# Kernel tuning notes

Measured on AMD Instinct MI355X. Metric: run time of the kernel, lower is better.

Reference implementation:

```python
import jax, jax.numpy as jnp
import numpy as np

N = 50000      # num nodes
NE = 20000     # num hyperedges
NNZ = 1000000  # incidence pairs |{(v,e)}|
F_IN = 128
HID = 64
NCLS = 40
NLAYER = 4
ALPHA = 0.1    # args.restart_alpha
LAMDA = 0.5


def setup_inputs() -> dict:
    key = jax.random.key(0)
    ks = jax.random.split(key, 8)
    x = jax.random.normal(ks[0], (N, F_IN), dtype=jnp.float32)
    vertex = jax.random.randint(ks[1], (NNZ,), 0, N, dtype=jnp.int32)
    edges = jax.random.randint(ks[2], (NNZ,), 0, NE, dtype=jnp.int32)
    W0 = jax.random.normal(ks[3], (F_IN, HID), dtype=jnp.float32) / np.float32(np.sqrt(F_IN))
    b0 = jnp.zeros((HID,), jnp.float32)
    Ws = jax.random.normal(ks[4], (NLAYER, HID, HID), dtype=jnp.float32) / np.float32(np.sqrt(HID))
    Wout = jax.random.normal(ks[5], (HID, NCLS), dtype=jnp.float32) / np.float32(np.sqrt(HID))
    bout = jnp.zeros((NCLS,), jnp.float32)
    return {"x": x, "vertex": vertex, "edges": edges, "W0": W0, "b0": b0,
            "Ws": Ws, "Wout": Wout, "bout": bout}


def _scatter_mean(src, idx, num_segments):
    s = jax.ops.segment_sum(src, idx, num_segments=num_segments)
    cnt = jax.ops.segment_sum(jnp.ones((idx.shape[0],), src.dtype), idx, num_segments=num_segments)
    return s / jnp.maximum(cnt, 1.0)[:, None]


def _normalize_l2(X):
    # torch: rownorm = X.detach().norm(dim=1, keepdim=True); scale = rownorm^-1; inf->0
    norm = jax.lax.stop_gradient(jnp.sqrt(jnp.sum(X * X, axis=-1, keepdims=True)))
    scale = jnp.where(norm > 0, 1.0 / jnp.maximum(norm, jnp.float32(1e-30)), 0.0)
    return X * scale


def reference(x, vertex, edges, W0, b0, Ws, Wout, bout):
    # input linear + relu (dropout = identity in eval mode)
    X = jax.nn.relu(x @ W0 + b0)
    X0 = X
    for i in range(NLAYER):
        beta = float(np.log(LAMDA / (i + 1) + 1.0))
        Xve = X[vertex]                       # gather node -> incidence  [NNZ, HID]
        Xe = _scatter_mean(Xve, edges, NE)    # scatter-mean -> hyperedge [NE, HID]
        Xev = Xe[edges]                       # gather hyperedge -> incidence [NNZ, HID]
        Xv = _scatter_mean(Xev, vertex, N)    # scatter-mean -> node      [N, HID]
        Xv = _normalize_l2(Xv)                # args.UniGNN_use_norm = True
        Xi = (1.0 - ALPHA) * Xv + ALPHA * X0
        X = jax.nn.relu((1.0 - beta) * Xi + beta * (Xi @ Ws[i]))
    return X @ Wout + bout
```

## Files before the change

### kernel.cpp

```cpp
#include <hip/hip_runtime.h>
#include <hip/hip_fp16.h>
#include <math.h>

#define N_NODES 50000
#define N_EDGES 20000
#define NNZ_C   1000000
#define F_IN    128
#define HID     64
#define NCLS    40
#define NLAYER  4
#define ALPHA   0.1f

#define ESHIFT  6
#define VSHIFT  7
#define NB_E    ((N_EDGES + 63) / 64)
#define NB_V    ((N_NODES + 127) / 128)
#define NB_TOT  (NB_E + NB_V)

typedef _Float16 f16x8 __attribute__((ext_vector_type(8)));
typedef float    f32x4 __attribute__((ext_vector_type(4)));

__global__ __launch_bounds__(256) void input_gemm(
    const float* __restrict__ x, const float* __restrict__ W0,
    const float* __restrict__ b0, _Float16* __restrict__ X0h,
    _Float16* __restrict__ Xh)
{
    int lane = threadIdx.x & 63;
    int wv   = threadIdx.x >> 6;
    int r16  = lane & 15;
    int kgrp = lane >> 4;
    f16x8 bf[4][4];
    #pragma unroll
    for (int n0 = 0; n0 < 4; ++n0)
        #pragma unroll
        for (int kh = 0; kh < 4; ++kh)
            #pragma unroll
            for (int j = 0; j < 8; ++j)
                bf[n0][kh][j] = (_Float16)W0[(kh * 32 + kgrp * 8 + j) * HID + n0 * 16 + r16];
    float bias[4];
    #pragma unroll
    for (int n0 = 0; n0 < 4; ++n0) bias[n0] = b0[n0 * 16 + r16];

    int nwaves = gridDim.x * 4;
    for (int t = blockIdx.x * 4 + wv; t < N_NODES / 16; t += nwaves) {
        int row0 = t * 16;
        const float* xp = x + (size_t)(row0 + r16) * F_IN + kgrp * 8;
        f16x8 a[4];
        #pragma unroll
        for (int kh = 0; kh < 4; ++kh) {
            float4 u0 = *(const float4*)(xp + kh * 32);
            float4 u1 = *(const float4*)(xp + kh * 32 + 4);
            a[kh][0] = (_Float16)u0.x; a[kh][1] = (_Float16)u0.y;
            a[kh][2] = (_Float16)u0.z; a[kh][3] = (_Float16)u0.w;
            a[kh][4] = (_Float16)u1.x; a[kh][5] = (_Float16)u1.y;
            a[kh][6] = (_Float16)u1.z; a[kh][7] = (_Float16)u1.w;
        }
        #pragma unroll
        for (int n0 = 0; n0 < 4; ++n0) {
            f32x4 acc = {0.f, 0.f, 0.f, 0.f};
            #pragma unroll
            for (int kh = 0; kh < 4; ++kh)
                acc = __builtin_amdgcn_mfma_f32_16x16x32_f16(a[kh], bf[n0][kh], acc, 0, 0, 0);
            #pragma unroll
            for (int r = 0; r < 4; ++r) {
                float y = acc[r] + bias[n0];
                y = y > 0.f ? y : 0.f;
                _Float16 h = (_Float16)y;
                size_t o = (size_t)(row0 + kgrp * 4 + r) * HID + n0 * 16 + r16;
                X0h[o] = h;
                Xh[o]  = h;
            }
        }
    }
}

__global__ __launch_bounds__(256) void make_wp(
    const float* __restrict__ Ws, _Float16* __restrict__ Wp,
    float be0, float be1, float be2, float be3)
{
    int l = blockIdx.x;
    float beta = (l == 0) ? be0 : (l == 1) ? be1 : (l == 2) ? be2 : be3;
    for (int i = threadIdx.x; i < HID * HID; i += 256) {
        int k = i >> 6, n = i & 63;
        float v = beta * Ws[l * HID * HID + i] + ((k == n) ? (1.f - beta) : 0.f);
        Wp[l * HID * HID + i] = (_Float16)v;
    }
}

__global__ __launch_bounds__(256) void bucket_hist(
    const int* __restrict__ vertex, const int* __restrict__ edges,
    int* __restrict__ gcnt)
{
    __shared__ int h[NB_TOT];
    int tid = threadIdx.x;
    for (int i = tid; i < NB_TOT; i += 256) h[i] = 0;
    __syncthreads();
    int base = blockIdx.x * 4096;
    int n = NNZ_C - base; if (n > 4096) n = 4096;
    for (int i = tid * 4; i < n; i += 1024) {
        int4 e4 = *(const int4*)(edges  + base + i);
        int4 v4 = *(const int4*)(vertex + base + i);
        atomicAdd(&h[e4.x >> ESHIFT], 1);
        atomicAdd(&h[e4.y >> ESHIFT], 1);
        atomicAdd(&h[e4.z >> ESHIFT], 1);
        atomicAdd(&h[e4.w >> ESHIFT], 1);
        atomicAdd(&h[NB_E + (v4.x >> VSHIFT)], 1);
        atomicAdd(&h[NB_E + (v4.y >> VSHIFT)], 1);
        atomicAdd(&h[NB_E + (v4.z >> VSHIFT)], 1);
        atomicAdd(&h[NB_E + (v4.w >> VSHIFT)], 1);
    }
    __syncthreads();
    for (int i = tid; i < NB_TOT; i += 256)
        if (h[i]) atomicAdd(&gcnt[i], h[i]);
}

__global__ __launch_bounds__(1024) void bucket_scan(
    const int* __restrict__ gcnt, int* __restrict__ boff_e,
    int* __restrict__ boff_v, int* __restrict__ curb)
{
    __shared__ int tmp[1024];
    int tid = threadIdx.x;
    int v = (tid < NB_TOT) ? gcnt[tid] : 0;
    tmp[tid] = v;
    __syncthreads();
    for (int d = 1; d < 1024; d <<= 1) {
        int t = (tid >= d) ? tmp[tid - d] : 0;
        __syncthreads();
        tmp[tid] += t;
        __syncthreads();
    }
    if (tid < NB_TOT) {
        int excl = tmp[tid] - v;
        int off = (tid < NB_E) ? excl : excl - NNZ_C;
        if (tid < NB_E) boff_e[tid] = off; else boff_v[tid - NB_E] = off;
        curb[tid] = off;
    }
    if (tid == 0) { boff_e[NB_E] = NNZ_C; boff_v[NB_V] = NNZ_C; }
}

__global__ __launch_bounds__(256) void bin_pass1_both(
    const int* __restrict__ vertex, const int* __restrict__ edges,
    int* __restrict__ curb,
    unsigned* __restrict__ binned_e,
    unsigned* __restrict__ binned_v)
{
    __shared__ int hist[NB_TOT];
    __shared__ int base[NB_TOT];
    int tid = threadIdx.x;
    int blk = blockIdx.x * 4096;
    int nh = NNZ_C - blk; if (nh > 4096) nh = 4096;
    for (int i = tid; i < NB_TOT; i += 256) hist[i] = 0;
    __syncthreads();
    for (int i = tid; i < nh; i += 256) {
        atomicAdd(&hist[edges[blk + i] >> ESHIFT], 1);
        atomicAdd(&hist[NB_E + (vertex[blk + i] >> VSHIFT)], 1);
    }
    __syncthreads();
    for (int i = tid; i < NB_TOT; i += 256) {
        int c = hist[i];
        base[i] = c ? atomicAdd(&curb[i], c) : 0;
        hist[i] = 0;
    }
    __syncthreads();
    for (int i = tid; i < nh; i += 256) {
        int e = edges[blk + i], v = vertex[blk + i];
        int be = e >> ESHIFT;
        int r  = atomicAdd(&hist[be], 1);
        binned_e[base[be] + r] = ((unsigned)e << 16) | (unsigned)v;
        int bv = NB_E + (v >> VSHIFT);
        int r2 = atomicAdd(&hist[bv], 1);
        binned_v[base[bv] + r2] = ((unsigned)v << 15) | (unsigned)e;
    }
}

__global__ __launch_bounds__(256) void bin_pass2f(
    const unsigned* __restrict__ binned, const int* __restrict__ boff,
    int shift, int kshift, int nkeys,
    int* __restrict__ off, float* __restrict__ inv, int* __restrict__ adj)
{
    __shared__ int lcnt[128];
    __shared__ int ts[128];
    __shared__ int lcur[128];
    int b  = blockIdx.x;
    int k0 = b << shift;
    int bs = 1 << shift;
    int kn = nkeys - k0; if (kn > bs) kn = bs;
    int tid = threadIdx.x;
    unsigned vmask = (1u << kshift) - 1u;
    if (tid < 128) lcnt[tid] = 0;
    __syncthreads();
    int beg = boff[b], end = boff[b + 1];
    for (int j = beg + tid; j < end; j += 256)
        atomicAdd(&lcnt[(int)(binned[j] >> kshift) - k0], 1);
    __syncthreads();
    int c = 0;
    if (tid < 128) { c = lcnt[tid]; ts[tid] = c; }
    __syncthreads();
    #pragma unroll
    for (int d = 1; d < 128; d <<= 1) {
        int t = 0;
        if (tid < 128 && tid >= d) t = ts[tid - d];
        __syncthreads();
        if (tid < 128) ts[tid] += t;
        __syncthreads();
    }
    if (tid < kn) {
        int pos = beg + ts[tid] - c;
        off[k0 + tid] = pos;
        inv[k0 + tid] = 1.0f / fmaxf((float)c, 1.0f);
        lcur[tid] = pos;
    }
    if (b == 0 && tid == 0) off[nkeys] = NNZ_C;
    __syncthreads();
    for (int j = beg + tid; j < end; j += 256) {
        unsigned p = binned[j];
        int k = (int)(p >> kshift) - k0;
        int v = (int)(p & vmask);
        adj[atomicAdd(&lcur[k], 1)] = v;
    }
}

__device__ __forceinline__ void gather_rows(
    const __half* __restrict__ src, const int* __restrict__ adj,
    int beg, int end, int lane, float acc[8])
{
    int g = lane >> 3, c = lane & 7;
    for (int j = beg; j < end; j += 64) {
        int nj = end - j; if (nj > 64) nj = 64;
        int myidx = (lane < nj) ? adj[j + lane] : 0;
        int idx[8];
        #pragma unroll
        for (int s = 0; s < 8; ++s)
            idx[s] = __shfl(myidx, ((s << 3) + g) & 63);
        #pragma unroll
        for (int s = 0; s < 8; ++s) {
            int r = (s << 3) + g;
            if (r < nj) {
                uint4 raw = ((const uint4*)(src + (size_t)idx[s] * HID))[c];
                union { uint4 u; __half2 h[4]; } U; U.u = raw;
                float2 f0 = __half22float2(U.h[0]);
                float2 f1 = __half22float2(U.h[1]);
                float2 f2 = __half22float2(U.h[2]);
                float2 f3 = __half22float2(U.h[3]);
                acc[0] += f0.x; acc[1] += f0.y;
                acc[2] += f1.x; acc[3] += f1.y;
                acc[4] += f2.x; acc[5] += f2.y;
                acc[6] += f3.x; acc[7] += f3.y;
            }
        }
    }
    #pragma unroll
    for (int q = 0; q < 8; ++q) {
        acc[q] += __shfl_xor(acc[q], 8);
        acc[q] += __shfl_xor(acc[q], 16);
        acc[q] += __shfl_xor(acc[q], 32);
    }
}

__global__ __launch_bounds__(256) void edge_gather(
    const __half* __restrict__ Xh, const int* __restrict__ adj_e,
    const int* __restrict__ off_e, const float* __restrict__ inv_e,
    __half* __restrict__ Xeh)
{
    int wid  = blockIdx.x * 4 + (threadIdx.x >> 6);
    int lane = threadIdx.x & 63;
    float acc[8] = {0.f,0.f,0.f,0.f,0.f,0.f,0.f,0.f};
    gather_rows(Xh, adj_e, off_e[wid], off_e[wid + 1], lane, acc);
    if ((lane >> 3) == 0) {
        float sc = inv_e[wid];
        union { uint4 u; __half2 h[4]; } O;
        O.h[0] = __floats2half2_rn(acc[0] * sc, acc[1] * sc);
        O.h[1] = __floats2half2_rn(acc[2] * sc, acc[3] * sc);
        O.h[2] = __floats2half2_rn(acc[4] * sc, acc[5] * sc);
        O.h[3] = __floats2half2_rn(acc[6] * sc, acc[7] * sc);
        ((uint4*)(Xeh + (size_t)wid * HID))[lane] = O.u;
    }
}

__global__ __launch_bounds__(256) void node_gather(
    const __half* __restrict__ Xeh, const int* __restrict__ adj_v,
    const int* __restrict__ off_v, const float* __restrict__ inv_v,
    const _Float16* __restrict__ X0h, _Float16* __restrict__ Xi)
{
    int wv   = threadIdx.x >> 6;
    int row  = blockIdx.x * 4 + wv;
    int lane = threadIdx.x & 63;
    float acc[8] = {0.f,0.f,0.f,0.f,0.f,0.f,0.f,0.f};
    gather_rows(Xeh, adj_v, off_v[row], off_v[row + 1], lane, acc);
    float scm = inv_v[row];
    float m[8]; float s = 0.f;
    #pragma unroll
    for (int q = 0; q < 8; ++q) { m[q] = acc[q] * scm; s += m[q] * m[q]; }
    s += __shfl_xor(s, 1);
    s += __shfl_xor(s, 2);
    s += __shfl_xor(s, 4);
    float norm  = sqrtf(s);
    float scale = norm > 0.f ? 1.0f / norm : 0.f;
    if ((lane >> 3) == 0) {
        union { f16x8 v; uint4 u; } I;
        I.u = *(const uint4*)(X0h + (size_t)row * HID + lane * 8);
        union { f16x8 v; uint4 u; } O;
        #pragma unroll
        for (int q = 0; q < 8; ++q)
            O.v[q] = (_Float16)((1.0f - ALPHA) * (m[q] * scale) + ALPHA * (float)I.v[q]);
        *(uint4*)(Xi + (size_t)row * HID + lane * 8) = O.u;
    }
}

__global__ __launch_bounds__(256) void layer_gemm(
    const _Float16* __restrict__ Xi, const _Float16* __restrict__ Wp,
    _Float16* __restrict__ Xh)
{
    int lane = threadIdx.x & 63;
    int wv   = threadIdx.x >> 6;
    int r16  = lane & 15;
    int kgrp = lane >> 4;
    f16x8 bf[4][2];
    #pragma unroll
    for (int n0 = 0; n0 < 4; ++n0)
        #pragma unroll
        for (int kh = 0; kh < 2; ++kh) {
            #pragma unroll
            for (int j = 0; j < 8; ++j)
                bf[n0][kh][j] = Wp[(kh * 32 + kgrp * 8 + j) * HID + n0 * 16 + r16];
        }
    int nwaves = gridDim.x * 4;
    for (int t = blockIdx.x * 4 + wv; t < N_NODES / 16; t += nwaves) {
        int row0 = t * 16;
        const _Float16* ap = Xi + (size_t)(row0 + r16) * HID + kgrp * 8;
        f16x8 a0 = *(const f16x8*)(ap);
        f16x8 a1 = *(const f16x8*)(ap + 32);
        #pragma unroll
        for (int n0 = 0; n0 < 4; ++n0) {
            f32x4 acc = {0.f, 0.f, 0.f, 0.f};
            acc = __builtin_amdgcn_mfma_f32_16x16x32_f16(a0, bf[n0][0], acc, 0, 0, 0);
            acc = __builtin_amdgcn_mfma_f32_16x16x32_f16(a1, bf[n0][1], acc, 0, 0, 0);
            #pragma unroll
            for (int r = 0; r < 4; ++r) {
                float y = acc[r] > 0.f ? acc[r] : 0.f;
                Xh[(size_t)(row0 + kgrp * 4 + r) * HID + n0 * 16 + r16] = (_Float16)y;
            }
        }
    }
}

__global__ __launch_bounds__(256) void out_gemm(
    const _Float16* __restrict__ Xh, const float* __restrict__ Wout,
    const float* __restrict__ bout, float* __restrict__ out)
{
    int lane = threadIdx.x & 63;
    int wv   = threadIdx.x >> 6;
    int r16  = lane & 15;
    int kgrp = lane >> 4;
    f16x8 bf[3][2];
    float bias[3];
    #pragma unroll
    for (int n0 = 0; n0 < 3; ++n0) {
        int col = n0 * 16 + r16;
        bias[n0] = (col < NCLS) ? bout[col] : 0.f;
        #pragma unroll
        for (int kh = 0; kh < 2; ++kh)
            #pragma unroll
            for (int j = 0; j < 8; ++j) {
                int k = kh * 32 + kgrp * 8 + j;
                bf[n0][kh][j] = (col < NCLS) ? (_Float16)Wout[k * NCLS + col] : (_Float16)0.f;
            }
    }
    int nwaves = gridDim.x * 4;
    for (int t = blockIdx.x * 4 + wv; t < N_NODES / 16; t += nwaves) {
        int row0 = t * 16;
        const _Float16* ap = Xh + (size_t)(row0 + r16) * HID + kgrp * 8;
        f16x8 a0 = *(const f16x8*)(ap);
        f16x8 a1 = *(const f16x8*)(ap + 32);
        #pragma unroll
        for (int n0 = 0; n0 < 3; ++n0) {
            f32x4 acc = {0.f, 0.f, 0.f, 0.f};
            acc = __builtin_amdgcn_mfma_f32_16x16x32_f16(a0, bf[n0][0], acc, 0, 0, 0);
            acc = __builtin_amdgcn_mfma_f32_16x16x32_f16(a1, bf[n0][1], acc, 0, 0, 0);
            int col = n0 * 16 + r16;
            if (col < NCLS) {
                #pragma unroll
                for (int r = 0; r < 4; ++r)
                    out[(size_t)(row0 + kgrp * 4 + r) * NCLS + col] = acc[r] + bias[n0];
            }
        }
    }
}

extern "C" void kernel_launch(void* const* d_in, const int* in_sizes, int n_in,
                              void* d_out, int out_size, void* d_ws, size_t ws_size,
                              hipStream_t stream)
{
    const float* x      = (const float*)d_in[0];
    const int*   vertex = (const int*)  d_in[1];
    const int*   edges  = (const int*)  d_in[2];
    const float* W0     = (const float*)d_in[3];
    const float* b0     = (const float*)d_in[4];
    const float* Ws     = (const float*)d_in[5];
    const float* Wout   = (const float*)d_in[6];
    const float* bout   = (const float*)d_in[7];
    float* out = (float*)d_out;

    char* ws = (char*)d_ws;
    unsigned* binned_e = (unsigned*)ws; ws += (size_t)NNZ_C * 4;
    unsigned* binned_v = (unsigned*)ws; ws += (size_t)NNZ_C * 4;
    _Float16*  X0h  = (_Float16*)ws;  ws += (size_t)N_NODES * HID * 2;
    _Float16*  Xh   = (_Float16*)ws;  ws += (size_t)N_NODES * HID * 2;
    _Float16*  Xi   = (_Float16*)ws;  ws += (size_t)N_NODES * HID * 2;
    __half*    Xeh  = (__half*)ws;    ws += (size_t)N_EDGES * HID * 2;
    _Float16*  Wp   = (_Float16*)ws;  ws += (size_t)NLAYER * HID * HID * 2;
    int*   adj_e  = (int*)ws;     ws += (size_t)NNZ_C * 4;
    int*   adj_v  = (int*)ws;     ws += (size_t)NNZ_C * 4;
    int*   off_e  = (int*)ws;     ws += (size_t)(N_EDGES + 1) * 4;
    int*   off_v  = (int*)ws;     ws += (size_t)(N_NODES + 1) * 4;
    float* inv_e  = (float*)ws;   ws += (size_t)N_EDGES * 4;
    float* inv_v  = (float*)ws;   ws += (size_t)N_NODES * 4;
    int*   gcnt   = (int*)ws;     ws += (size_t)NB_TOT * 4;
    int*   boff_e = (int*)ws;     ws += (size_t)(NB_E + 1) * 4;
    int*   boff_v = (int*)ws;     ws += (size_t)(NB_V + 1) * 4;
    int*   curb   = (int*)ws;     ws += (size_t)NB_TOT * 4;

    const int p1_grid = (NNZ_C + 4095) / 4096;

    hipMemsetAsync(gcnt, 0, (size_t)NB_TOT * 4, stream);
    bucket_hist<<<p1_grid, 256, 0, stream>>>(vertex, edges, gcnt);
    bucket_scan<<<1, 1024, 0, stream>>>(gcnt, boff_e, boff_v, curb);
    bin_pass1_both<<<p1_grid, 256, 0, stream>>>(vertex, edges, curb, binned_e, binned_v);
    bin_pass2f<<<NB_E, 256, 0, stream>>>(binned_e, boff_e, ESHIFT, 16, N_EDGES, off_e, inv_e, adj_e);
    bin_pass2f<<<NB_V, 256, 0, stream>>>(binned_v, boff_v, VSHIFT, 15, N_NODES, off_v, inv_v, adj_v);

    float be0 = logf(0.5f / 1.f + 1.0f);
    float be1 = logf(0.5f / 2.f + 1.0f);
    float be2 = logf(0.5f / 3.f + 1.0f);
    float be3 = logf(0.5f / 4.f + 1.0f);
    make_wp<<<NLAYER, 256, 0, stream>>>(Ws, Wp, be0, be1, be2, be3);

    input_gemm<<<391, 256, 0, stream>>>(x, W0, b0, X0h, Xh);

    for (int l = 0; l < NLAYER; ++l) {
        edge_gather<<<N_EDGES / 4, 256, 0, stream>>>((__half*)Xh, adj_e, off_e, inv_e, Xeh);
        node_gather<<<N_NODES / 4, 256, 0, stream>>>(
            Xeh, adj_v, off_v, inv_v, X0h, Xi);
        layer_gemm<<<391, 256, 0, stream>>>(Xi, Wp + (size_t)l * HID * HID, Xh);
    }

    out_gemm<<<391, 256, 0, stream>>>(Xh, Wout, bout, out);
}
```

Measured before the change: 285.7 us.

## Fuse node gather, normalization and layer GEMM into one MFMA kernel

```diff
diff --git a/kernel.cpp b/kernel.cpp
--- a/kernel.cpp
+++ b/kernel.cpp
@@ -22,8 +22,7 @@
 
 __global__ __launch_bounds__(256) void input_gemm(
     const float* __restrict__ x, const float* __restrict__ W0,
-    const float* __restrict__ b0, _Float16* __restrict__ X0h,
-    _Float16* __restrict__ Xh)
+    const float* __restrict__ b0, _Float16* __restrict__ X0h)
 {
     int lane = threadIdx.x & 63;
     int wv   = threadIdx.x >> 6;
@@ -65,10 +64,7 @@
             for (int r = 0; r < 4; ++r) {
                 float y = acc[r] + bias[n0];
                 y = y > 0.f ? y : 0.f;
-                _Float16 h = (_Float16)y;
-                size_t o = (size_t)(row0 + kgrp * 4 + r) * HID + n0 * 16 + r16;
-                X0h[o] = h;
-                Xh[o]  = h;
+                X0h[(size_t)(row0 + kgrp * 4 + r) * HID + n0 * 16 + r16] = (_Float16)y;
             }
         }
     }
@@ -220,35 +216,34 @@
     }
 }
 
-__device__ __forceinline__ void gather_rows(
-    const __half* __restrict__ src, const int* __restrict__ adj,
-    int beg, int end, int lane, float acc[8])
+__device__ __forceinline__ void process_chunk(
+    const __half* __restrict__ src, int myidx, int nj, int lane, float acc[8])
 {
     int g = lane >> 3, c = lane & 7;
-    for (int j = beg; j < end; j += 64) {
-        int nj = end - j; if (nj > 64) nj = 64;
-        int myidx = (lane < nj) ? adj[j + lane] : 0;
-        int idx[8];
-        #pragma unroll
-        for (int s = 0; s < 8; ++s)
-            idx[s] = __shfl(myidx, ((s << 3) + g) & 63);
-        #pragma unroll
-        for (int s = 0; s < 8; ++s) {
-            int r = (s << 3) + g;
-            if (r < nj) {
-                uint4 raw = ((const uint4*)(src + (size_t)idx[s] * HID))[c];
-                union { uint4 u; __half2 h[4]; } U; U.u = raw;
-                float2 f0 = __half22float2(U.h[0]);
-                float2 f1 = __half22float2(U.h[1]);
-                float2 f2 = __half22float2(U.h[2]);
-                float2 f3 = __half22float2(U.h[3]);
-                acc[0] += f0.x; acc[1] += f0.y;
-                acc[2] += f1.x; acc[3] += f1.y;
-                acc[4] += f2.x; acc[5] += f2.y;
-                acc[6] += f3.x; acc[7] += f3.y;
-            }
-        }
-    }
+    int idx[8];
+    #pragma unroll
+    for (int s = 0; s < 8; ++s)
+        idx[s] = __shfl(myidx, ((s << 3) + g) & 63);
+    #pragma unroll
+    for (int s = 0; s < 8; ++s) {
+        int r = (s << 3) + g;
+        if (r < nj) {
+            uint4 raw = ((const uint4*)(src + (size_t)idx[s] * HID))[c];
+            union { uint4 u; __half2 h[4]; } U; U.u = raw;
+            float2 f0 = __half22float2(U.h[0]);
+            float2 f1 = __half22float2(U.h[1]);
+            float2 f2 = __half22float2(U.h[2]);
+            float2 f3 = __half22float2(U.h[3]);
+            acc[0] += f0.x; acc[1] += f0.y;
+            acc[2] += f1.x; acc[3] += f1.y;
+            acc[4] += f2.x; acc[5] += f2.y;
+            acc[6] += f3.x; acc[7] += f3.y;
+        }
+    }
+}
+
+__device__ __forceinline__ void reduce_groups(float acc[8])
+{
     #pragma unroll
     for (int q = 0; q < 8; ++q) {
         acc[q] += __shfl_xor(acc[q], 8);
@@ -264,8 +259,14 @@
 {
     int wid  = blockIdx.x * 4 + (threadIdx.x >> 6);
     int lane = threadIdx.x & 63;
+    int beg = off_e[wid], end = off_e[wid + 1];
     float acc[8] = {0.f,0.f,0.f,0.f,0.f,0.f,0.f,0.f};
-    gather_rows(Xh, adj_e, off_e[wid], off_e[wid + 1], lane, acc);
+    for (int j = beg; j < end; j += 64) {
+        int nj = end - j; if (nj > 64) nj = 64;
+        int myidx = (lane < nj) ? adj_e[j + lane] : 0;
+        process_chunk(Xh, myidx, nj, lane, acc);
+    }
+    reduce_groups(acc);
     if ((lane >> 3) == 0) {
         float sc = inv_e[wid];
         union { uint4 u; __half2 h[4]; } O;
@@ -277,70 +278,81 @@
     }
 }
 
-__global__ __launch_bounds__(256) void node_gather(
+__global__ __launch_bounds__(256) void node_fused_mfma(
     const __half* __restrict__ Xeh, const int* __restrict__ adj_v,
     const int* __restrict__ off_v, const float* __restrict__ inv_v,
-    const _Float16* __restrict__ X0h, _Float16* __restrict__ Xi)
-{
+    const _Float16* __restrict__ X0h, const _Float16* __restrict__ Wp,
+    _Float16* __restrict__ Xh)
+{
+    __shared__ _Float16 xi[16][72];
     int wv   = threadIdx.x >> 6;
-    int row  = blockIdx.x * 4 + wv;
     int lane = threadIdx.x & 63;
-    float acc[8] = {0.f,0.f,0.f,0.f,0.f,0.f,0.f,0.f};
-    gather_rows(Xeh, adj_v, off_v[row], off_v[row + 1], lane, acc);
-    float scm = inv_v[row];
-    float m[8]; float s = 0.f;
-    #pragma unroll
-    for (int q = 0; q < 8; ++q) { m[q] = acc[q] * scm; s += m[q] * m[q]; }
-    s += __shfl_xor(s, 1);
-    s += __shfl_xor(s, 2);
-    s += __shfl_xor(s, 4);
-    float norm  = sqrtf(s);
-    float scale = norm > 0.f ? 1.0f / norm : 0.f;
-    if ((lane >> 3) == 0) {
-        union { f16x8 v; uint4 u; } I;
-        I.u = *(const uint4*)(X0h + (size_t)row * HID + lane * 8);
-        union { f16x8 v; uint4 u; } O;
-        #pragma unroll
-        for (int q = 0; q < 8; ++q)
-            O.v[q] = (_Float16)((1.0f - ALPHA) * (m[q] * scale) + ALPHA * (float)I.v[q]);
-        *(uint4*)(Xi + (size_t)row * HID + lane * 8) = O.u;
-    }
-}
-
-__global__ __launch_bounds__(256) void layer_gemm(
-    const _Float16* __restrict__ Xi, const _Float16* __restrict__ Wp,
-    _Float16* __restrict__ Xh)
-{
-    int lane = threadIdx.x & 63;
-    int wv   = threadIdx.x >> 6;
     int r16  = lane & 15;
     int kgrp = lane >> 4;
-    f16x8 bf[4][2];
-    #pragma unroll
-    for (int n0 = 0; n0 < 4; ++n0)
-        #pragma unroll
-        for (int kh = 0; kh < 2; ++kh) {
+    int base = blockIdx.x * 16 + wv * 4;
+
+    f16x8 bfA, bfB;
+    #pragma unroll
+    for (int j = 0; j < 8; ++j) {
+        bfA[j] = Wp[(kgrp * 8 + j) * HID + wv * 16 + r16];
+        bfB[j] = Wp[(32 + kgrp * 8 + j) * HID + wv * 16 + r16];
+    }
+
+    int beg[4], deg[4], myidx[4];
+    #pragma unroll
+    for (int i = 0; i < 4; ++i) {
+        beg[i] = off_v[base + i];
+        deg[i] = off_v[base + i + 1] - beg[i];
+    }
+    #pragma unroll
+    for (int i = 0; i < 4; ++i) {
+        int nj = deg[i] < 64 ? deg[i] : 64;
+        myidx[i] = (lane < nj) ? adj_v[beg[i] + lane] : 0;
+    }
+
+    #pragma unroll
+    for (int i = 0; i < 4; ++i) {
+        int row = base + i;
+        float acc[8] = {0.f,0.f,0.f,0.f,0.f,0.f,0.f,0.f};
+        int nj0 = deg[i] < 64 ? deg[i] : 64;
+        process_chunk(Xeh, myidx[i], nj0, lane, acc);
+        for (int j = beg[i] + 64; j < beg[i] + deg[i]; j += 64) {
+            int nj = beg[i] + deg[i] - j; if (nj > 64) nj = 64;
+            int mi = (lane < nj) ? adj_v[j + lane] : 0;
+            process_chunk(Xeh, mi, nj, lane, acc);
+        }
+        reduce_groups(acc);
+        float scm = inv_v[row];
+        float m[8]; float s = 0.f;
+        #pragma unroll
+        for (int q = 0; q < 8; ++q) { m[q] = acc[q] * scm; s += m[q] * m[q]; }
+        s += __shfl_xor(s, 1);
+        s += __shfl_xor(s, 2);
+        s += __shfl_xor(s, 4);
+        float norm  = sqrtf(s);
+        float scale = norm > 0.f ? 1.0f / norm : 0.f;
+        if ((lane >> 3) == 0) {
+            union { f16x8 v; uint4 u; } I;
+            I.u = *(const uint4*)(X0h + (size_t)row * HID + lane * 8);
+            union { f16x8 v; uint4 u; } O;
             #pragma unroll
-            for (int j = 0; j < 8; ++j)
-                bf[n0][kh][j] = Wp[(kh * 32 + kgrp * 8 + j) * HID + n0 * 16 + r16];
-        }
-    int nwaves = gridDim.x * 4;
-    for (int t = blockIdx.x * 4 + wv; t < N_NODES / 16; t += nwaves) {
-        int row0 = t * 16;
-        const _Float16* ap = Xi + (size_t)(row0 + r16) * HID + kgrp * 8;
-        f16x8 a0 = *(const f16x8*)(ap);
-        f16x8 a1 = *(const f16x8*)(ap + 32);
-        #pragma unroll
-        for (int n0 = 0; n0 < 4; ++n0) {
-            f32x4 acc = {0.f, 0.f, 0.f, 0.f};
-            acc = __builtin_amdgcn_mfma_f32_16x16x32_f16(a0, bf[n0][0], acc, 0, 0, 0);
-            acc = __builtin_amdgcn_mfma_f32_16x16x32_f16(a1, bf[n0][1], acc, 0, 0, 0);
-            #pragma unroll
-            for (int r = 0; r < 4; ++r) {
-                float y = acc[r] > 0.f ? acc[r] : 0.f;
-                Xh[(size_t)(row0 + kgrp * 4 + r) * HID + n0 * 16 + r16] = (_Float16)y;
-            }
-        }
+            for (int q = 0; q < 8; ++q)
+                O.v[q] = (_Float16)((1.0f - ALPHA) * (m[q] * scale) + ALPHA * (float)I.v[q]);
+            *(uint4*)&xi[wv * 4 + i][lane * 8] = O.u;
+        }
+    }
+    __syncthreads();
+
+    f16x8 a0 = *(const f16x8*)&xi[r16][kgrp * 8];
+    f16x8 a1 = *(const f16x8*)&xi[r16][kgrp * 8 + 32];
+    f32x4 acc = {0.f, 0.f, 0.f, 0.f};
+    acc = __builtin_amdgcn_mfma_f32_16x16x32_f16(a0, bfA, acc, 0, 0, 0);
+    acc = __builtin_amdgcn_mfma_f32_16x16x32_f16(a1, bfB, acc, 0, 0, 0);
+    int rowbase = blockIdx.x * 16;
+    #pragma unroll
+    for (int r = 0; r < 4; ++r) {
+        float y = acc[r] > 0.f ? acc[r] : 0.f;
+        Xh[(size_t)(rowbase + kgrp * 4 + r) * HID + wv * 16 + r16] = (_Float16)y;
     }
 }
 
@@ -406,7 +418,6 @@
     unsigned* binned_v = (unsigned*)ws; ws += (size_t)NNZ_C * 4;
     _Float16*  X0h  = (_Float16*)ws;  ws += (size_t)N_NODES * HID * 2;
     _Float16*  Xh   = (_Float16*)ws;  ws += (size_t)N_NODES * HID * 2;
-    _Float16*  Xi   = (_Float16*)ws;  ws += (size_t)N_NODES * HID * 2;
     __half*    Xeh  = (__half*)ws;    ws += (size_t)N_EDGES * HID * 2;
     _Float16*  Wp   = (_Float16*)ws;  ws += (size_t)NLAYER * HID * HID * 2;
     int*   adj_e  = (int*)ws;     ws += (size_t)NNZ_C * 4;
@@ -435,13 +446,13 @@
     float be3 = logf(0.5f / 4.f + 1.0f);
     make_wp<<<NLAYER, 256, 0, stream>>>(Ws, Wp, be0, be1, be2, be3);
 
-    input_gemm<<<391, 256, 0, stream>>>(x, W0, b0, X0h, Xh);
+    input_gemm<<<391, 256, 0, stream>>>(x, W0, b0, X0h);
 
     for (int l = 0; l < NLAYER; ++l) {
-        edge_gather<<<N_EDGES / 4, 256, 0, stream>>>((__half*)Xh, adj_e, off_e, inv_e, Xeh);
-        node_gather<<<N_NODES / 4, 256, 0, stream>>>(
-            Xeh, adj_v, off_v, inv_v, X0h, Xi);
-        layer_gemm<<<391, 256, 0, stream>>>(Xi, Wp + (size_t)l * HID * HID, Xh);
+        const _Float16* Xin = (l == 0) ? X0h : Xh;
+        edge_gather<<<N_EDGES / 4, 256, 0, stream>>>((const __half*)Xin, adj_e, off_e, inv_e, Xeh);
+        node_fused_mfma<<<N_NODES / 16, 256, 0, stream>>>(
+            Xeh, adj_v, off_v, inv_v, X0h, Wp + (size_t)l * HID * HID, Xh);
     }
 
     out_gemm<<<391, 256, 0, stream>>>(Xh, Wout, bout, out);
```

Result: slower. 303.4 us (+6.2%).
